# Performance work log

Hardware: AMD Instinct MI355X
Metric: run time of the kernel (lower is better)

The kernel has to match this reference:

```python
import jax, jax.numpy as jnp
import numpy as np

B, T, VOCAB_SZ, N_SPK = 64, 1024, 34, 128
D_TXT, D_SPK, H, N_MELS = 512, 64, 256, 80


def _lstm_params(key, in_dim, hid):
    k1, k2, k3, k4 = jax.random.split(key, 4)
    s = 1.0 / np.sqrt(hid)
    Wih = jax.random.uniform(k1, (4 * hid, in_dim), jnp.float32, -s, s)
    Whh = jax.random.uniform(k2, (4 * hid, hid), jnp.float32, -s, s)
    bih = jax.random.uniform(k3, (4 * hid,), jnp.float32, -s, s)
    bhh = jax.random.uniform(k4, (4 * hid,), jnp.float32, -s, s)
    return Wih, Whh, bih, bhh


def setup_inputs() -> dict:
    key = jax.random.key(0)
    ks = jax.random.split(key, 10)
    text_seq = jax.random.randint(ks[0], (B, T), 0, VOCAB_SZ)
    mel_spectrogram = jax.random.normal(ks[1], (B, T, N_MELS), jnp.float32)
    speaker_id = jax.random.randint(ks[2], (B,), 0, N_SPK)
    emb_text = jax.random.normal(ks[3], (VOCAB_SZ, D_TXT), jnp.float32)
    emb_text = emb_text.at[0].set(0.0)  # padding_idx=0
    emb_spk = jax.random.normal(ks[4], (N_SPK, D_SPK), jnp.float32)
    Wih_f, Whh_f, bih_f, bhh_f = _lstm_params(ks[5], D_TXT + D_SPK, H)
    Wih_b, Whh_b, bih_b, bhh_b = _lstm_params(ks[6], D_TXT + D_SPK, H)
    Wih_d, _Whh_d, bih_d, bhh_d = _lstm_params(ks[7], N_MELS + 2 * H, H)
    s = 1.0 / np.sqrt(H)
    Wfc = jax.random.uniform(ks[8], (N_MELS, H), jnp.float32, -s, s)
    bfc = jax.random.uniform(ks[9], (N_MELS,), jnp.float32, -s, s)
    return dict(text_seq=text_seq, mel_spectrogram=mel_spectrogram, speaker_id=speaker_id,
                emb_text=emb_text, emb_spk=emb_spk,
                Wih_f=Wih_f, Whh_f=Whh_f, bih_f=bih_f, bhh_f=bhh_f,
                Wih_b=Wih_b, Whh_b=Whh_b, bih_b=bih_b, bhh_b=bhh_b,
                Wih_d=Wih_d, bih_d=bih_d, bhh_d=bhh_d, Wfc=Wfc, bfc=bfc)


def _lstm_scan(xs, Wih, Whh, bih, bhh, reverse=False):
    # xs: [T, B, D] -> hs: [T, B, H] (PyTorch gate order i,f,g,o)
    nB, hid = xs.shape[1], Whh.shape[1]
    bias = bih + bhh
    def step(carry, x):
        h, c = carry
        g = x @ Wih.T + h @ Whh.T + bias
        i, f, gg, o = jnp.split(g, 4, axis=-1)
        c = jax.nn.sigmoid(f) * c + jax.nn.sigmoid(i) * jnp.tanh(gg)
        h = jax.nn.sigmoid(o) * jnp.tanh(c)
        return (h, c), h
    init = (jnp.zeros((nB, hid), xs.dtype), jnp.zeros((nB, hid), xs.dtype))
    _, hs = jax.lax.scan(step, init, xs, reverse=reverse)
    return hs


def reference(text_seq, mel_spectrogram, speaker_id, emb_text, emb_spk,
              Wih_f, Whh_f, bih_f, bhh_f, Wih_b, Whh_b, bih_b, bhh_b,
              Wih_d, bih_d, bhh_d, Wfc, bfc):
    text_embed = emb_text[text_seq]                       # [B, T, 512]
    spk = jnp.broadcast_to(emb_spk[speaker_id][:, None, :],
                           (text_seq.shape[0], text_seq.shape[1], emb_spk.shape[1]))
    enc_in = jnp.concatenate([text_embed, spk], axis=-1)  # [B, T, 576]
    xs = jnp.transpose(enc_in, (1, 0, 2))                 # time-major [T, B, 576]
    h_fwd = _lstm_scan(xs, Wih_f, Whh_f, bih_f, bhh_f)
    h_bwd = _lstm_scan(xs, Wih_b, Whh_b, bih_b, bhh_b, reverse=True)
    enc_out = jnp.concatenate([h_fwd, h_bwd], axis=-1)    # [T, B, 512]

    max_len = min(mel_spectrogram.shape[1], enc_out.shape[0])
    # Decoder: hidden state is reset (None) every step in the original, so
    # c = sigmoid(i)*tanh(g), h = sigmoid(o)*tanh(c); Whh contributes nothing.
    dbias = bih_d + bhh_d
    def dstep(prev_mel, e_t):
        x = jnp.concatenate([prev_mel, e_t], axis=-1)     # [B, 592]
        g = x @ Wih_d.T + dbias
        i, f, gg, o = jnp.split(g, 4, axis=-1)
        c = jax.nn.sigmoid(i) * jnp.tanh(gg)
        h = jax.nn.sigmoid(o) * jnp.tanh(c)
        out = h @ Wfc.T + bfc
        return out, out
    _, outs = jax.lax.scan(dstep, mel_spectrogram[:, 0, :], enc_out[: max_len - 1])
    return jnp.transpose(outs, (1, 0, 2))                 # [B, max_len-1, 80]
```

## Files before the change

### kernel.cpp

```cpp
#include <hip/hip_runtime.h>
#include <hip/hip_fp16.h>
#include <stdint.h>

#define T_SEQ 1024
#define NB    64
#define VOCAB 34
#define NSPK  128
#define DTXT  512
#define HID   256
#define NMEL  80
#define GROWS 1024
#define DROWS 768

typedef _Float16 f16;
typedef _Float16 f16x2 __attribute__((ext_vector_type(2)));

__device__ __forceinline__ float fdot2f(uint32_t a, uint32_t b, float c) {
  return __builtin_amdgcn_fdot2(__builtin_bit_cast(f16x2, a),
                                __builtin_bit_cast(f16x2, b), c, false);
}
__device__ __forceinline__ float sigm(float x) { return 1.0f / (1.0f + __expf(-x)); }
__device__ __forceinline__ float tanhf_fast(float x) {
  float e = __expf(2.0f * x);
  return 1.0f - 2.0f / (e + 1.0f);
}


__global__ void k_tp(const float* __restrict__ Wf, const float* __restrict__ Wb,
                     const float* __restrict__ emb_text, float* __restrict__ TP) {
  int blk = blockIdx.x; int dir = blk / VOCAB; int v = blk - dir * VOCAB;
  const float* W = dir ? Wb : Wf;
  const float* e = emb_text + (size_t)v * DTXT;
  for (int r = threadIdx.x; r < GROWS; r += 256) {
    const float* wr = W + (size_t)r * 576;
    float a0 = 0, a1 = 0, a2 = 0, a3 = 0;
    for (int d = 0; d < DTXT; d += 4) {
      a0 += e[d] * wr[d];     a1 += e[d+1] * wr[d+1];
      a2 += e[d+2] * wr[d+2]; a3 += e[d+3] * wr[d+3];
    }
    TP[(size_t)(dir * VOCAB + v) * GROWS + r] = (a0 + a1) + (a2 + a3);
  }
}

__global__ void k_sp(const float* __restrict__ Wf, const float* __restrict__ Wb,
                     const float* __restrict__ bihf, const float* __restrict__ bhhf,
                     const float* __restrict__ bihb, const float* __restrict__ bhhb,
                     const float* __restrict__ emb_spk, float* __restrict__ SP) {
  int blk = blockIdx.x; int dir = blk >> 7; int s = blk & 127;
  const float* W  = dir ? Wb : Wf;
  const float* bi = dir ? bihb : bihf;
  const float* bh = dir ? bhhb : bhhf;
  const float* e  = emb_spk + (size_t)s * 64;
  for (int r = threadIdx.x; r < GROWS; r += 256) {
    const float* wr = W + (size_t)r * 576 + 512;
    float acc = bi[r] + bh[r];
    for (int d = 0; d < 64; ++d) acc += e[d] * wr[d];
    SP[(size_t)(dir * NSPK + s) * GROWS + r] = acc;
  }
}

__global__ void k_whh(const float* __restrict__ Whhf, const float* __restrict__ Whhb,
                      f16* __restrict__ WhhH) {
  int idx = blockIdx.x * 256 + threadIdx.x;
  if (idx < 2 * GROWS * HID) {
    int dir = idx >> 18; int rem = idx & (GROWS * HID - 1);
    WhhH[idx] = (f16)(dir ? Whhb[rem] : Whhf[rem]);
  }
}

__global__ void k_decw(const float* __restrict__ Wih_d, const float* __restrict__ bih_d,
                       const float* __restrict__ bhh_d,
                       f16* __restrict__ WmH, f16* __restrict__ WdH, float* __restrict__ dbias) {
  int r = blockIdx.x;
  int src = (r < 256) ? r : (r + 256);
  const float* w = Wih_d + (size_t)src * 592;
  for (int k = threadIdx.x; k < 592; k += 256) {
    float v = w[k];
    if (k < 80) WmH[(size_t)r * 80 + k] = (f16)v;
    else        WdH[(size_t)r * 512 + (k - 80)] = (f16)v;
  }
  if (threadIdx.x == 0) dbias[r] = bih_d[src] + bhh_d[src];
}

__global__ void k_misc(const float* __restrict__ Wfc, f16* __restrict__ WfcH) {
  int idx = blockIdx.x * 256 + threadIdx.x;
  if (idx < NMEL * HID) WfcH[idx] = (f16)Wfc[idx];
}

__launch_bounds__(512, 2)
__global__ void k_enc(const int* __restrict__ text_seq, const int* __restrict__ speaker_id,
                      const float* __restrict__ TP, const float* __restrict__ SP,
                      const uint32_t* __restrict__ WhhH_dw,
                      f16* __restrict__ Hh) {
  __shared__ __align__(16) uint4 wtail[16 * 512];
  __shared__ __align__(16) uint32_t hbuf[2][128];
  __shared__ float pp[4][256];
  __shared__ int tseq[T_SEQ];

  int wg = blockIdx.x;
  int dir = wg >> 6, b = wg & 63;
  int tid = threadIdx.x;
  int u = tid & 255, kh = tid >> 8;

  uint4 w0[12], w1[12], w2[12], w3[12];
  {
    const uint4* p0 = (const uint4*)(WhhH_dw + ((size_t)(dir << 10) + u      ) * 128 + (kh << 6));
    const uint4* p1 = (const uint4*)(WhhH_dw + ((size_t)(dir << 10) + u + 256) * 128 + (kh << 6));
    const uint4* p2 = (const uint4*)(WhhH_dw + ((size_t)(dir << 10) + u + 512) * 128 + (kh << 6));
    const uint4* p3 = (const uint4*)(WhhH_dw + ((size_t)(dir << 10) + u + 768) * 128 + (kh << 6));
    #pragma unroll
    for (int i = 0; i < 12; ++i) { w0[i] = p0[i]; w1[i] = p1[i]; w2[i] = p2[i]; w3[i] = p3[i]; }
    #pragma unroll
    for (int j = 0; j < 4; ++j) {
      wtail[(0 * 4 + j) * 512 + tid] = p0[12 + j];
      wtail[(1 * 4 + j) * 512 + tid] = p1[12 + j];
      wtail[(2 * 4 + j) * 512 + tid] = p2[12 + j];
      wtail[(3 * 4 + j) * 512 + tid] = p3[12 + j];
    }
  }
  for (int i = tid; i < T_SEQ; i += 512) tseq[i] = text_seq[b * T_SEQ + i];
  if (tid < 128) hbuf[0][tid] = 0u;
  float sp0 = 0, sp1 = 0, sp2 = 0, sp3 = 0;
  if (kh == 0) {
    int spk = speaker_id[b];
    sp0 = SP[(size_t)(dir * NSPK + spk) * GROWS + u];
    sp1 = SP[(size_t)(dir * NSPK + spk) * GROWS + u + 256];
    sp2 = SP[(size_t)(dir * NSPK + spk) * GROWS + u + 512];
    sp3 = SP[(size_t)(dir * NSPK + spk) * GROWS + u + 768];
  }
  const float* TPd = TP + (size_t)dir * VOCAB * GROWS;
  float c_state = 0.0f;
  __syncthreads();

  float x0 = 0, x1 = 0, x2 = 0, x3 = 0;
  if (kh == 0) {
    int v = tseq[dir ? (T_SEQ - 1) : 0];
    x0 = TPd[(size_t)v * GROWS + u];
    x1 = TPd[(size_t)v * GROWS + u + 256];
    x2 = TPd[(size_t)v * GROWS + u + 512];
    x3 = TPd[(size_t)v * GROWS + u + 768];
  }

  float h_keep = 0.0f; int t_keep = 0;
  for (int n = 0; n < T_SEQ; ++n) {
    int t = dir ? (T_SEQ - 1 - n) : n;
    float xn0 = 0, xn1 = 0, xn2 = 0, xn3 = 0;
    if (kh == 0) {
      if (n > 0)
        Hh[((size_t)(dir * T_SEQ + t_keep) * NB + b) * HID + u] = (f16)h_keep;
      int tn = dir ? (T_SEQ - 2 - n) : (n + 1);
      tn = tn < 0 ? 0 : (tn > T_SEQ - 1 ? T_SEQ - 1 : tn);
      int vn = tseq[tn];
      xn0 = TPd[(size_t)vn * GROWS + u];
      xn1 = TPd[(size_t)vn * GROWS + u + 256];
      xn2 = TPd[(size_t)vn * GROWS + u + 512];
      xn3 = TPd[(size_t)vn * GROWS + u + 768];
    }

    float i0 = 0, i1 = 0, f0 = 0, f1 = 0, g0 = 0, g1 = 0, o0 = 0, o1 = 0;
    const uint4* h4 = ((const uint4*)hbuf[n & 1]) + (kh << 4);
    #pragma unroll
    for (int c = 0; c < 12; ++c) {
      uint4 hv = h4[c];
      i0 = fdot2f(w0[c].x, hv.x, i0); f0 = fdot2f(w1[c].x, hv.x, f0);
      g0 = fdot2f(w2[c].x, hv.x, g0); o0 = fdot2f(w3[c].x, hv.x, o0);
      i1 = fdot2f(w0[c].y, hv.y, i1); f1 = fdot2f(w1[c].y, hv.y, f1);
      g1 = fdot2f(w2[c].y, hv.y, g1); o1 = fdot2f(w3[c].y, hv.y, o1);
      i0 = fdot2f(w0[c].z, hv.z, i0); f0 = fdot2f(w1[c].z, hv.z, f0);
      g0 = fdot2f(w2[c].z, hv.z, g0); o0 = fdot2f(w3[c].z, hv.z, o0);
      i1 = fdot2f(w0[c].w, hv.w, i1); f1 = fdot2f(w1[c].w, hv.w, f1);
      g1 = fdot2f(w2[c].w, hv.w, g1); o1 = fdot2f(w3[c].w, hv.w, o1);
    }
    #pragma unroll
    for (int j = 0; j < 4; ++j) {
      uint4 hv = h4[12 + j];
      uint4 t0v = wtail[(0 * 4 + j) * 512 + tid];
      uint4 t1v = wtail[(1 * 4 + j) * 512 + tid];
      uint4 t2v = wtail[(2 * 4 + j) * 512 + tid];
      uint4 t3v = wtail[(3 * 4 + j) * 512 + tid];
      i0 = fdot2f(t0v.x, hv.x, i0); f0 = fdot2f(t1v.x, hv.x, f0);
      g0 = fdot2f(t2v.x, hv.x, g0); o0 = fdot2f(t3v.x, hv.x, o0);
      i1 = fdot2f(t0v.y, hv.y, i1); f1 = fdot2f(t1v.y, hv.y, f1);
      g1 = fdot2f(t2v.y, hv.y, g1); o1 = fdot2f(t3v.y, hv.y, o1);
      i0 = fdot2f(t0v.z, hv.z, i0); f0 = fdot2f(t1v.z, hv.z, f0);
      g0 = fdot2f(t2v.z, hv.z, g0); o0 = fdot2f(t3v.z, hv.z, o0);
      i1 = fdot2f(t0v.w, hv.w, i1); f1 = fdot2f(t1v.w, hv.w, f1);
      g1 = fdot2f(t2v.w, hv.w, g1); o1 = fdot2f(t3v.w, hv.w, o1);
    }
    if (kh == 1) {
      pp[0][u] = i0 + i1;
      pp[1][u] = f0 + f1;
      pp[2][u] = g0 + g1;
      pp[3][u] = o0 + o1;
    }
    __syncthreads();

    if (kh == 0) {
      float gi = (i0 + i1) + pp[0][u] + x0 + sp0;
      float gf = (f0 + f1) + pp[1][u] + x1 + sp1;
      float gg = (g0 + g1) + pp[2][u] + x2 + sp2;
      float go = (o0 + o1) + pp[3][u] + x3 + sp3;
      c_state = sigm(gf) * c_state + sigm(gi) * tanhf_fast(gg);
      float h = sigm(go) * tanhf_fast(c_state);
      ((f16*)hbuf[(n + 1) & 1])[u] = (f16)h;
      h_keep = h; t_keep = t;
      x0 = xn0; x1 = xn1; x2 = xn2; x3 = xn3;
    }
    __syncthreads();
  }
  if (kh == 0)
    Hh[((size_t)(dir * T_SEQ + t_keep) * NB + b) * HID + u] = (f16)h_keep;
}

__launch_bounds__(256, 4)
__global__ void k_eproj(const uint32_t* __restrict__ Hdw, const uint32_t* __restrict__ WdH_dw,
                        const float* __restrict__ dbias, f16* __restrict__ E) {
  __shared__ __align__(16) uint32_t Asm[64][68];
  __shared__ __align__(16) uint32_t Wsm[64][68];
  int nt = blockIdx.x % 12;
  int t  = blockIdx.x / 12;
  int n0 = nt * 64;
  int tid = threadIdx.x;
  int i = tid & 15, j = tid >> 4;
  float acc[4][4] = {};

  for (int ch = 0; ch < 4; ++ch) {
    int dirc = ch >> 1, koff = (ch & 1) * 64;
    {
      int bb = tid >> 2, p = tid & 3;
      const uint32_t* asrc = Hdw + ((size_t)(dirc * T_SEQ + t) * NB + bb) * 128 + koff + p * 4;
      const uint32_t* wsrc = WdH_dw + (size_t)(n0 + bb) * 256 + ch * 64 + p * 4;
      #pragma unroll
      for (int q = 0; q < 4; ++q) {
        *(uint4*)(&Asm[bb][p * 4 + q * 16]) = *(const uint4*)(asrc + q * 16);
        *(uint4*)(&Wsm[bb][p * 4 + q * 16]) = *(const uint4*)(wsrc + q * 16);
      }
    }
    __syncthreads();
    #pragma unroll
    for (int kc = 0; kc < 16; ++kc) {
      uint4 av[4], wv4[4];
      #pragma unroll
      for (int r = 0; r < 4; ++r) av[r]  = *(const uint4*)&Asm[i + 16 * r][kc * 4];
      #pragma unroll
      for (int s = 0; s < 4; ++s) wv4[s] = *(const uint4*)&Wsm[j + 16 * s][kc * 4];
      #pragma unroll
      for (int r = 0; r < 4; ++r)
        #pragma unroll
        for (int s = 0; s < 4; ++s) {
          acc[r][s] = fdot2f(av[r].x, wv4[s].x, acc[r][s]);
          acc[r][s] = fdot2f(av[r].y, wv4[s].y, acc[r][s]);
          acc[r][s] = fdot2f(av[r].z, wv4[s].z, acc[r][s]);
          acc[r][s] = fdot2f(av[r].w, wv4[s].w, acc[r][s]);
        }
    }
    __syncthreads();
  }
  #pragma unroll
  for (int r = 0; r < 4; ++r)
    #pragma unroll
    for (int s = 0; s < 4; ++s) {
      int m = i + 16 * r;
      int n = n0 + j + 16 * s;
      E[((size_t)t * NB + m) * DROWS + n] = (f16)(acc[r][s] + dbias[n]);
    }
}

__launch_bounds__(512, 2)
__global__ void k_dec(const float* __restrict__ mel, const f16* __restrict__ E,
                      const uint32_t* __restrict__ WmH_dw, const uint32_t* __restrict__ WfcH_dw,
                      const float* __restrict__ bfc, float* __restrict__ out) {
  __shared__ __align__(16) uint32_t pm[40];
  __shared__ __align__(16) uint32_t h_sm[128];
  __shared__ float pp[3][256];
  __shared__ float partial[80][4];
  __shared__ __align__(16) uint4 Ebuf[2][16 * 96];

  int b = blockIdx.x;
  int tid = threadIdx.x;
  int u = tid & 255, kh = tid >> 8;

  uint4 wm0[5], wm1[5], wm2[5];
  {
    const uint4* p0 = (const uint4*)(WmH_dw + (size_t)(u      ) * 40) + kh * 5;
    const uint4* p1 = (const uint4*)(WmH_dw + (size_t)(u + 256) * 40) + kh * 5;
    const uint4* p2 = (const uint4*)(WmH_dw + (size_t)(u + 512) * 40) + kh * 5;
    #pragma unroll
    for (int k = 0; k < 5; ++k) { wm0[k] = p0[k]; wm1[k] = p1[k]; wm2[k] = p2[k]; }
  }
  int fr = (tid < 320) ? (tid >> 2) : 0;
  int q  = tid & 3;
  uint4 wfc[8];
  {
    const uint4* wp = (const uint4*)(WfcH_dw + (size_t)fr * 128) + q * 8;
    #pragma unroll
    for (int k = 0; k < 8; ++k) wfc[k] = wp[k];
  }
  float bfcv = bfc[tid < NMEL ? tid : 0];
  if (tid < 40) {
    float m0 = mel[(size_t)b * T_SEQ * NMEL + 2 * tid];
    float m1 = mel[(size_t)b * T_SEQ * NMEL + 2 * tid + 1];
    f16x2 v; v[0] = (f16)m0; v[1] = (f16)m1;
    pm[tid] = __builtin_bit_cast(uint32_t, v);
  }

  int srow = tid >> 5, scol = tid & 31;
  {
    const uint4* src = (const uint4*)(E + ((size_t)srow * NB + b) * DROWS);
    Ebuf[0][srow * 96 + scol     ] = src[scol];
    Ebuf[0][srow * 96 + scol + 32] = src[scol + 32];
    Ebuf[0][srow * 96 + scol + 64] = src[scol + 64];
  }
  __syncthreads();

  float o_keep = 0.0f;
  for (int t = 0; t < T_SEQ - 1; ++t) {
    int w = t >> 4, s = t & 15;
    if (t > 0 && tid < NMEL)
      out[((size_t)b * (T_SEQ - 1) + (t - 1)) * NMEL + tid] = o_keep;
    uint4 st0, st1, st2;
    bool do_stage = (s == 0) && (w < 63);
    if (do_stage) {
      int rr = (w + 1) * 16 + srow; if (rr > T_SEQ - 2) rr = T_SEQ - 2;
      const uint4* src = (const uint4*)(E + ((size_t)rr * NB + b) * DROWS);
      st0 = src[scol]; st1 = src[scol + 32]; st2 = src[scol + 64];
    }

    float a0 = 0, a1 = 0, a2 = 0;
    const uint4* pm4 = ((const uint4*)pm) + kh * 5;
    #pragma unroll
    for (int k = 0; k < 5; ++k) {
      uint4 hp = pm4[k];
      a0 = fdot2f(wm0[k].x, hp.x, a0); a1 = fdot2f(wm1[k].x, hp.x, a1); a2 = fdot2f(wm2[k].x, hp.x, a2);
      a0 = fdot2f(wm0[k].y, hp.y, a0); a1 = fdot2f(wm1[k].y, hp.y, a1); a2 = fdot2f(wm2[k].y, hp.y, a2);
      a0 = fdot2f(wm0[k].z, hp.z, a0); a1 = fdot2f(wm1[k].z, hp.z, a1); a2 = fdot2f(wm2[k].z, hp.z, a2);
      a0 = fdot2f(wm0[k].w, hp.w, a0); a1 = fdot2f(wm1[k].w, hp.w, a1); a2 = fdot2f(wm2[k].w, hp.w, a2);
    }
    if (kh == 1) { pp[0][u] = a0; pp[1][u] = a1; pp[2][u] = a2; }
    __syncthreads();

    if (kh == 0) {
      const f16* Erow = (const f16*)&Ebuf[w & 1][s * 96];
      float gi = a0 + pp[0][u] + (float)Erow[u];
      float gg = a1 + pp[1][u] + (float)Erow[u + 256];
      float go = a2 + pp[2][u] + (float)Erow[u + 512];
      float cc = sigm(gi) * tanhf_fast(gg);
      float h  = sigm(go) * tanhf_fast(cc);
      ((f16*)h_sm)[u] = (f16)h;
    }
    if (do_stage) {
      Ebuf[(w + 1) & 1][srow * 96 + scol     ] = st0;
      Ebuf[(w + 1) & 1][srow * 96 + scol + 32] = st1;
      Ebuf[(w + 1) & 1][srow * 96 + scol + 64] = st2;
    }
    __syncthreads();

    if (tid < 320) {
      const uint4* hrow = ((const uint4*)h_sm) + q * 8;
      float s0 = 0, s1 = 0, s2 = 0, s3 = 0;
      #pragma unroll
      for (int kk = 0; kk < 8; ++kk) {
        uint4 hq = hrow[kk];
        s0 = fdot2f(wfc[kk].x, hq.x, s0); s1 = fdot2f(wfc[kk].y, hq.y, s1);
        s2 = fdot2f(wfc[kk].z, hq.z, s2); s3 = fdot2f(wfc[kk].w, hq.w, s3);
      }
      partial[fr][q] = (s0 + s1) + (s2 + s3);
    }
    __syncthreads();

    if (tid < NMEL) {
      float o = ((partial[tid][0] + partial[tid][1]) +
                 (partial[tid][2] + partial[tid][3])) + bfcv;
      o_keep = o;
      ((f16*)pm)[tid] = (f16)o;
    }
    __syncthreads();
  }
  if (tid < NMEL)
    out[((size_t)b * (T_SEQ - 1) + (T_SEQ - 2)) * NMEL + tid] = o_keep;
}

extern "C" void kernel_launch(void* const* d_in, const int* in_sizes, int n_in,
                              void* d_out, int out_size, void* d_ws, size_t ws_size,
                              hipStream_t stream) {
  const int*   text_seq   = (const int*)d_in[0];
  const float* mel        = (const float*)d_in[1];
  const int*   speaker_id = (const int*)d_in[2];
  const float* emb_text   = (const float*)d_in[3];
  const float* emb_spk    = (const float*)d_in[4];
  const float* Wih_f = (const float*)d_in[5];
  const float* Whh_f = (const float*)d_in[6];
  const float* bih_f = (const float*)d_in[7];
  const float* bhh_f = (const float*)d_in[8];
  const float* Wih_b = (const float*)d_in[9];
  const float* Whh_b = (const float*)d_in[10];
  const float* bih_b = (const float*)d_in[11];
  const float* bhh_b = (const float*)d_in[12];
  const float* Wih_d = (const float*)d_in[13];
  const float* bih_d = (const float*)d_in[14];
  const float* bhh_d = (const float*)d_in[15];
  const float* Wfc   = (const float*)d_in[16];
  const float* bfc   = (const float*)d_in[17];
  float* out = (float*)d_out;

  char* base = (char*)d_ws;
  size_t off = 0;
  auto take = [&](size_t n) -> char* {
    off = (off + 255) & ~(size_t)255;
    char* r = base + off;
    off += n;
    return r;
  };
  float*        TP    = (float*)take((size_t)2 * VOCAB * GROWS * 4);
  float*        SP    = (float*)take((size_t)2 * NSPK * GROWS * 4);
  f16*          WhhH  = (f16*)take((size_t)2 * GROWS * HID * 2);
  f16*          WmH   = (f16*)take((size_t)DROWS * 80 * 2);
  f16*          WdH   = (f16*)take((size_t)DROWS * 512 * 2);
  f16*          WfcH  = (f16*)take((size_t)NMEL * HID * 2);
  float*        dbias = (float*)take((size_t)DROWS * 4);
  f16*          Hh    = (f16*)take((size_t)2 * T_SEQ * NB * HID * 2);
  f16*          E     = (f16*)take((size_t)(T_SEQ - 1) * NB * DROWS * 2);
  if (off > ws_size) return;

  k_tp  <<<2 * VOCAB, 256, 0, stream>>>(Wih_f, Wih_b, emb_text, TP);
  k_sp  <<<2 * NSPK, 256, 0, stream>>>(Wih_f, Wih_b, bih_f, bhh_f, bih_b, bhh_b, emb_spk, SP);
  k_whh <<<2048, 256, 0, stream>>>(Whh_f, Whh_b, WhhH);
  k_decw<<<DROWS, 256, 0, stream>>>(Wih_d, bih_d, bhh_d, WmH, WdH, dbias);
  k_misc<<<80, 256, 0, stream>>>(Wfc, WfcH);
  k_enc <<<128, 512, 0, stream>>>(text_seq, speaker_id, TP, SP,
                                  (const uint32_t*)WhhH, Hh);
  k_eproj<<<(T_SEQ - 1) * 12, 256, 0, stream>>>((const uint32_t*)Hh,
                                                (const uint32_t*)WdH, dbias, E);
  k_dec <<<NB, 512, 0, stream>>>(mel, E, (const uint32_t*)WmH,
                                 (const uint32_t*)WfcH, bfc, out);
}
```

Before: 3.319 ms.

## Use MFMA for encoder projection GEMM and keep more recurrent weights in registers

The encoder-output projection kernel replaces its fdot2 register-tiled inner product with 16x16x32 f16 MFMA instructions, one 16-row strip per wave across four 16-column tiles. The epilogue is rewritten to the MFMA accumulator layout, with the bias hoisted into registers. Separately, the recurrent encoder kernel holds 14 of 16 weight chunks in registers instead of 12, halving the LDS tail it rereads every step. The aim is to cut ALU time in the projection and LDS traffic in the serial recurrence, at the cost of higher register pressure that could cause spills.

```diff
diff --git a/kernel.cpp b/kernel.cpp
--- a/kernel.cpp
+++ b/kernel.cpp
@@ -14,6 +14,8 @@
 
 typedef _Float16 f16;
 typedef _Float16 f16x2 __attribute__((ext_vector_type(2)));
+typedef _Float16 v8h __attribute__((ext_vector_type(8)));
+typedef float v4f __attribute__((ext_vector_type(4)));
 
 __device__ __forceinline__ float fdot2f(uint32_t a, uint32_t b, float c) {
   return __builtin_amdgcn_fdot2(__builtin_bit_cast(f16x2, a),
@@ -92,7 +94,7 @@
                       const float* __restrict__ TP, const float* __restrict__ SP,
                       const uint32_t* __restrict__ WhhH_dw,
                       f16* __restrict__ Hh) {
-  __shared__ __align__(16) uint4 wtail[16 * 512];
+  __shared__ __align__(16) uint4 wtail[8 * 512];
   __shared__ __align__(16) uint32_t hbuf[2][128];
   __shared__ float pp[4][256];
   __shared__ int tseq[T_SEQ];
@@ -102,20 +104,20 @@
   int tid = threadIdx.x;
   int u = tid & 255, kh = tid >> 8;
 
-  uint4 w0[12], w1[12], w2[12], w3[12];
+  uint4 w0[14], w1[14], w2[14], w3[14];
   {
     const uint4* p0 = (const uint4*)(WhhH_dw + ((size_t)(dir << 10) + u      ) * 128 + (kh << 6));
     const uint4* p1 = (const uint4*)(WhhH_dw + ((size_t)(dir << 10) + u + 256) * 128 + (kh << 6));
     const uint4* p2 = (const uint4*)(WhhH_dw + ((size_t)(dir << 10) + u + 512) * 128 + (kh << 6));
     const uint4* p3 = (const uint4*)(WhhH_dw + ((size_t)(dir << 10) + u + 768) * 128 + (kh << 6));
     #pragma unroll
-    for (int i = 0; i < 12; ++i) { w0[i] = p0[i]; w1[i] = p1[i]; w2[i] = p2[i]; w3[i] = p3[i]; }
-    #pragma unroll
-    for (int j = 0; j < 4; ++j) {
-      wtail[(0 * 4 + j) * 512 + tid] = p0[12 + j];
-      wtail[(1 * 4 + j) * 512 + tid] = p1[12 + j];
-      wtail[(2 * 4 + j) * 512 + tid] = p2[12 + j];
-      wtail[(3 * 4 + j) * 512 + tid] = p3[12 + j];
+    for (int i = 0; i < 14; ++i) { w0[i] = p0[i]; w1[i] = p1[i]; w2[i] = p2[i]; w3[i] = p3[i]; }
+    #pragma unroll
+    for (int j = 0; j < 2; ++j) {
+      wtail[(0 * 2 + j) * 512 + tid] = p0[14 + j];
+      wtail[(1 * 2 + j) * 512 + tid] = p1[14 + j];
+      wtail[(2 * 2 + j) * 512 + tid] = p2[14 + j];
+      wtail[(3 * 2 + j) * 512 + tid] = p3[14 + j];
     }
   }
   for (int i = tid; i < T_SEQ; i += 512) tseq[i] = text_seq[b * T_SEQ + i];
@@ -160,7 +162,7 @@
     float i0 = 0, i1 = 0, f0 = 0, f1 = 0, g0 = 0, g1 = 0, o0 = 0, o1 = 0;
     const uint4* h4 = ((const uint4*)hbuf[n & 1]) + (kh << 4);
     #pragma unroll
-    for (int c = 0; c < 12; ++c) {
+    for (int c = 0; c < 14; ++c) {
       uint4 hv = h4[c];
       i0 = fdot2f(w0[c].x, hv.x, i0); f0 = fdot2f(w1[c].x, hv.x, f0);
       g0 = fdot2f(w2[c].x, hv.x, g0); o0 = fdot2f(w3[c].x, hv.x, o0);
@@ -172,12 +174,12 @@
       g1 = fdot2f(w2[c].w, hv.w, g1); o1 = fdot2f(w3[c].w, hv.w, o1);
     }
     #pragma unroll
-    for (int j = 0; j < 4; ++j) {
-      uint4 hv = h4[12 + j];
-      uint4 t0v = wtail[(0 * 4 + j) * 512 + tid];
-      uint4 t1v = wtail[(1 * 4 + j) * 512 + tid];
-      uint4 t2v = wtail[(2 * 4 + j) * 512 + tid];
-      uint4 t3v = wtail[(3 * 4 + j) * 512 + tid];
+    for (int j = 0; j < 2; ++j) {
+      uint4 hv = h4[14 + j];
+      uint4 t0v = wtail[(0 * 2 + j) * 512 + tid];
+      uint4 t1v = wtail[(1 * 2 + j) * 512 + tid];
+      uint4 t2v = wtail[(2 * 2 + j) * 512 + tid];
+      uint4 t3v = wtail[(3 * 2 + j) * 512 + tid];
       i0 = fdot2f(t0v.x, hv.x, i0); f0 = fdot2f(t1v.x, hv.x, f0);
       g0 = fdot2f(t2v.x, hv.x, g0); o0 = fdot2f(t3v.x, hv.x, o0);
       i1 = fdot2f(t0v.y, hv.y, i1); f1 = fdot2f(t1v.y, hv.y, f1);
@@ -221,8 +223,10 @@
   int t  = blockIdx.x / 12;
   int n0 = nt * 64;
   int tid = threadIdx.x;
-  int i = tid & 15, j = tid >> 4;
-  float acc[4][4] = {};
+  int wave = tid >> 6, lane = tid & 63;
+  int lr = lane & 15, lg = lane >> 4;
+
+  v4f acc0 = {0,0,0,0}, acc1 = {0,0,0,0}, acc2 = {0,0,0,0}, acc3 = {0,0,0,0};
 
   for (int ch = 0; ch < 4; ++ch) {
     int dirc = ch >> 1, koff = (ch & 1) * 64;
@@ -238,32 +242,33 @@
     }
     __syncthreads();
     #pragma unroll
-    for (int kc = 0; kc < 16; ++kc) {
-      uint4 av[4], wv4[4];
-      #pragma unroll
-      for (int r = 0; r < 4; ++r) av[r]  = *(const uint4*)&Asm[i + 16 * r][kc * 4];
-      #pragma unroll
-      for (int s = 0; s < 4; ++s) wv4[s] = *(const uint4*)&Wsm[j + 16 * s][kc * 4];
-      #pragma unroll
-      for (int r = 0; r < 4; ++r)
-        #pragma unroll
-        for (int s = 0; s < 4; ++s) {
-          acc[r][s] = fdot2f(av[r].x, wv4[s].x, acc[r][s]);
-          acc[r][s] = fdot2f(av[r].y, wv4[s].y, acc[r][s]);
-          acc[r][s] = fdot2f(av[r].z, wv4[s].z, acc[r][s]);
-          acc[r][s] = fdot2f(av[r].w, wv4[s].w, acc[r][s]);
-        }
-    }
-    __syncthreads();
-  }
+    for (int sub = 0; sub < 4; ++sub) {
+      v8h af = __builtin_bit_cast(v8h, *(const uint4*)&Asm[wave * 16 + lr][sub * 16 + lg * 4]);
+      v8h b0 = __builtin_bit_cast(v8h, *(const uint4*)&Wsm[ 0 + lr][sub * 16 + lg * 4]);
+      v8h b1 = __builtin_bit_cast(v8h, *(const uint4*)&Wsm[16 + lr][sub * 16 + lg * 4]);
+      v8h b2 = __builtin_bit_cast(v8h, *(const uint4*)&Wsm[32 + lr][sub * 16 + lg * 4]);
+      v8h b3 = __builtin_bit_cast(v8h, *(const uint4*)&Wsm[48 + lr][sub * 16 + lg * 4]);
+      acc0 = __builtin_amdgcn_mfma_f32_16x16x32_f16(af, b0, acc0, 0, 0, 0);
+      acc1 = __builtin_amdgcn_mfma_f32_16x16x32_f16(af, b1, acc1, 0, 0, 0);
+      acc2 = __builtin_amdgcn_mfma_f32_16x16x32_f16(af, b2, acc2, 0, 0, 0);
+      acc3 = __builtin_amdgcn_mfma_f32_16x16x32_f16(af, b3, acc3, 0, 0, 0);
+    }
+    __syncthreads();
+  }
+
+  float db0 = dbias[n0 +  0 + lr];
+  float db1 = dbias[n0 + 16 + lr];
+  float db2 = dbias[n0 + 32 + lr];
+  float db3 = dbias[n0 + 48 + lr];
   #pragma unroll
-  for (int r = 0; r < 4; ++r)
-    #pragma unroll
-    for (int s = 0; s < 4; ++s) {
-      int m = i + 16 * r;
-      int n = n0 + j + 16 * s;
-      E[((size_t)t * NB + m) * DROWS + n] = (f16)(acc[r][s] + dbias[n]);
-    }
+  for (int reg = 0; reg < 4; ++reg) {
+    int m = wave * 16 + lg * 4 + reg;
+    f16* Erow = E + ((size_t)t * NB + m) * DROWS + n0;
+    Erow[ 0 + lr] = (f16)(acc0[reg] + db0);
+    Erow[16 + lr] = (f16)(acc1[reg] + db1);
+    Erow[32 + lr] = (f16)(acc2[reg] + db2);
+    Erow[48 + lr] = (f16)(acc3[reg] + db3);
+  }
 }
 
 __launch_bounds__(512, 2)
```

Result: faster. 3.023 ms (-8.9%).
